# Kernel tuning notes

Measured on AMD Instinct MI355X. Metric: run time of the kernel, lower is better.

The kernel has to match this reference:

```python
import jax, jax.numpy as jnp
import numpy as np

B, T, D, H, K = 8, 4096, 768, 12, 64
EPS_WKV = 1e-9
EPS_GN = 1e-5


def setup_inputs() -> dict:
    key = jax.random.key(0)
    ks = jax.random.split(key, 12)
    x = jax.random.normal(ks[0], (B, T, D), jnp.float32)
    # linear projection weights (torch nn.Linear stores [out, in]; y = x @ W.T)
    W_r = jax.random.normal(ks[1], (D, D), jnp.float32) * 0.02
    W_k = jax.random.normal(ks[2], (D, D), jnp.float32) * 0.02
    W_v = jax.random.normal(ks[3], (D, D), jnp.float32) * 0.02
    W_o = jax.random.normal(ks[4], (D, D), jnp.float32) * 0.02
    time_mix_r = jax.random.uniform(ks[5], (D,), jnp.float32)
    time_mix_k = jax.random.uniform(ks[6], (D,), jnp.float32)
    time_mix_v = jax.random.uniform(ks[7], (D,), jnp.float32)
    # around the module's init values (time_decay ~ -0.075, time_first ~ 0.15 at layer 6/12)
    time_decay = -0.075 + 0.1 * jax.random.normal(ks[8], (H, K), jnp.float32)
    time_first = 0.15 + 0.1 * jax.random.normal(ks[9], (H, K), jnp.float32)
    gn_weight = jnp.ones((D,), jnp.float32)
    gn_bias = jnp.zeros((D,), jnp.float32)
    return {
        "x": x,
        "time_mix_r": time_mix_r, "time_mix_k": time_mix_k, "time_mix_v": time_mix_v,
        "time_decay": time_decay, "time_first": time_first,
        "W_r": W_r, "W_k": W_k, "W_v": W_v, "W_o": W_o,
        "gn_weight": gn_weight, "gn_bias": gn_bias,
    }


def reference(x, time_mix_r, time_mix_k, time_mix_v, time_decay, time_first,
              W_r, W_k, W_v, W_o, gn_weight, gn_bias):
    Bx, Tx, Dx = x.shape
    Hx, Kx = time_decay.shape
    # token-shift: previous timestep (zero-initialized state)
    x_prev = jnp.concatenate([jnp.zeros_like(x[:, :1]), x[:, :-1]], axis=1)
    xr = x * time_mix_r + x_prev * (1.0 - time_mix_r)
    xk = x * time_mix_k + x_prev * (1.0 - time_mix_k)
    xv = x * time_mix_v + x_prev * (1.0 - time_mix_v)
    r = jax.nn.sigmoid(xr @ W_r.T).reshape(Bx, Tx, Hx, Kx)
    k = (xk @ W_k.T).reshape(Bx, Tx, Hx, Kx)
    v = (xv @ W_v.T).reshape(Bx, Tx, Hx, Kx)

    w = jnp.exp(-jnp.exp(time_decay))   # [H,K] decay per channel
    eu = jnp.exp(time_first)            # [H,K] bonus for current token

    def step(carry, kv_t):
        num, den = carry                # each [B,H,K]
        k_t, v_t = kv_t                 # each [B,H,K]
        ek = jnp.exp(k_t)
        wkv = (num + eu * ek * v_t) / (den + eu * ek + EPS_WKV)
        return (num * w + ek * v_t, den * w + ek), wkv

    k_tm = jnp.moveaxis(k, 1, 0)        # [T,B,H,K]
    v_tm = jnp.moveaxis(v, 1, 0)
    init = (jnp.zeros((Bx, Hx, Kx), x.dtype), jnp.zeros((Bx, Hx, Kx), x.dtype))
    _, wkv = jax.lax.scan(step, init, (k_tm, v_tm))
    out = jnp.moveaxis(wkv, 0, 1)       # [B,T,H,K]

    y = r * out                         # [B,T,H,K]
    # torch GroupNorm(H, D) on [B, D, T]: normalize each group over (K channels x T steps)
    mean = y.mean(axis=(1, 3), keepdims=True)
    var = y.var(axis=(1, 3), keepdims=True)
    y = (y - mean) * jax.lax.rsqrt(var + EPS_GN)
    y = y * gn_weight.reshape(1, 1, Hx, Kx) + gn_bias.reshape(1, 1, Hx, Kx)
    return y.reshape(Bx, Tx, Dx) @ W_o.T
```

## Files before the change

kernel.cpp:

```cpp
#include <hip/hip_runtime.h>
#include <hip/hip_bf16.h>
#include <cstdint>

#define B_ 8
#define T_ 4096
#define D_ 768
#define H_ 12
#define M_ (B_*T_)
#define CHUNKS 256
#define CLEN 16
#define WELEM (D_*D_)
#define NCH (B_*H_*64)

typedef __attribute__((ext_vector_type(8))) short bf16x8;
typedef __attribute__((ext_vector_type(4))) float f32x4;

static __device__ __forceinline__ unsigned short f2bf(float f) {
  __hip_bfloat16 h = __float2bfloat16(f);
  return __builtin_bit_cast(unsigned short, h);
}
static __device__ __forceinline__ float bf2f(unsigned short u) {
  unsigned v = ((unsigned)u) << 16;
  return __builtin_bit_cast(float, v);
}

static __device__ __forceinline__ void async16(const void* g, void* l) {
  __builtin_amdgcn_global_load_lds(
      (const __attribute__((address_space(1))) unsigned int*)g,
      (__attribute__((address_space(3))) unsigned int*)l, 16, 0, 0);
}

__global__ __launch_bounds__(256) void zero_out_kernel(float* __restrict__ out, size_t n4) {
  size_t gid = (size_t)blockIdx.x * 256 + threadIdx.x;
  if (gid < n4) *(float4*)(out + gid * 4) = make_float4(0.f, 0.f, 0.f, 0.f);
}

__global__ __launch_bounds__(256) void mix_kernel(
    const float* __restrict__ x, const float* __restrict__ tmr,
    const float* __restrict__ tmk, const float* __restrict__ tmv,
    unsigned short* __restrict__ xr, unsigned short* __restrict__ xk,
    unsigned short* __restrict__ xv) {
  size_t gid = (size_t)blockIdx.x * 256 + threadIdx.x;
  size_t idx4 = gid * 4;
  int d = (int)(idx4 % D_);
  size_t row = idx4 / D_;
  int t = (int)(row & (T_ - 1));
  float4 xc = *(const float4*)(x + idx4);
  float4 xp = make_float4(0.f, 0.f, 0.f, 0.f);
  if (t > 0) xp = *(const float4*)(x + idx4 - D_);
  float4 mr = *(const float4*)(tmr + d);
  float4 mk = *(const float4*)(tmk + d);
  float4 mv = *(const float4*)(tmv + d);
  ushort4 orr, okk, ovv;
  orr.x = f2bf(xc.x*mr.x + xp.x*(1.f-mr.x));
  orr.y = f2bf(xc.y*mr.y + xp.y*(1.f-mr.y));
  orr.z = f2bf(xc.z*mr.z + xp.z*(1.f-mr.z));
  orr.w = f2bf(xc.w*mr.w + xp.w*(1.f-mr.w));
  okk.x = f2bf(xc.x*mk.x + xp.x*(1.f-mk.x));
  okk.y = f2bf(xc.y*mk.y + xp.y*(1.f-mk.y));
  okk.z = f2bf(xc.z*mk.z + xp.z*(1.f-mk.z));
  okk.w = f2bf(xc.w*mk.w + xp.w*(1.f-mk.w));
  ovv.x = f2bf(xc.x*mv.x + xp.x*(1.f-mv.x));
  ovv.y = f2bf(xc.y*mv.y + xp.y*(1.f-mv.y));
  ovv.z = f2bf(xc.z*mv.z + xp.z*(1.f-mv.z));
  ovv.w = f2bf(xc.w*mv.w + xp.w*(1.f-mv.w));
  *(ushort4*)(xr + idx4) = orr;
  *(ushort4*)(xk + idx4) = okk;
  *(ushort4*)(xv + idx4) = ovv;
}

__global__ __launch_bounds__(256) void wconv_kernel(
    const float* __restrict__ a, const float* __restrict__ b,
    const float* __restrict__ c, unsigned short* __restrict__ o) {
  size_t gid = (size_t)blockIdx.x * 256 + threadIdx.x;
  size_t idx4 = gid * 4;
  size_t mi = idx4 / WELEM;
  size_t off = idx4 % WELEM;
  const float* src = (mi == 0) ? a : (mi == 1) ? b : c;
  float4 v = *(const float4*)(src + off);
  ushort4 u;
  u.x = f2bf(v.x); u.y = f2bf(v.y); u.z = f2bf(v.z); u.w = f2bf(v.w);
  *(ushort4*)(o + idx4) = u;
}

template<int ACT, int OBF, int BIAS>
__global__ __launch_bounds__(256, 3) void gemm_nt(
    const unsigned short* __restrict__ A,
    const unsigned short* __restrict__ Bw,
    void* __restrict__ Cv, const float* __restrict__ bias2) {
  __shared__ __align__(16) unsigned short smem[128 * 128];
  const int tid = threadIdx.x;
  const int wave = tid >> 6, lane = tid & 63;
  const int quad = lane >> 4, l16 = lane & 15;

  int nwg = gridDim.x * gridDim.y;
  int lin = blockIdx.y * gridDim.x + blockIdx.x;
  int q = nwg >> 3, r = nwg & 7;
  int xcd = lin & 7, off = lin >> 3;
  int swz = (xcd < r ? xcd * (q + 1) : r * (q + 1) + (xcd - r) * q) + off;
  const int m0 = (swz / gridDim.x) * 128;
  const int n0 = (swz % gridDim.x) * 128;
  const int wm = (wave & 1) * 64, wn = (wave >> 1) * 64;
  const int bb = m0 >> 12;
  const unsigned short* Bp = BIAS ? Bw + (size_t)bb * WELEM : Bw;

  auto stage = [&](int buf, int kb) {
    unsigned short* Ls = smem + buf * (128 * 64);
#pragma unroll
    for (int j = 0; j < 2; ++j) {
      int chunk = j * 256 + tid;
      int row = chunk >> 2, slot = chunk & 3;
      int ks = slot ^ ((row >> 1) & 3);
      async16(A  + ((size_t)(m0 + row)) * D_ + kb + ks * 8, &Ls[chunk * 8]);
      async16(Bp + ((size_t)(n0 + row)) * D_ + kb + ks * 8, &Ls[128 * 32 + chunk * 8]);
    }
  };

  f32x4 acc[4][4] = {};
  const int NT = D_ / 32;

  stage(0, 0);
  __syncthreads();
  int cur = 0;
  for (int t = 0; t < NT; ++t) {
    if (t + 1 < NT) stage(cur ^ 1, (t + 1) * 32);
    const unsigned short* As = smem + cur * (128 * 64);
    const unsigned short* Bs = As + 128 * 32;
    bf16x8 a[4], b[4];
#pragma unroll
    for (int i = 0; i < 4; ++i) {
      int ra = wm + i * 16 + l16;
      a[i] = *(const bf16x8*)&As[ra * 32 + ((quad ^ ((ra >> 1) & 3)) * 8)];
      int rb = wn + i * 16 + l16;
      b[i] = *(const bf16x8*)&Bs[rb * 32 + ((quad ^ ((rb >> 1) & 3)) * 8)];
    }
#pragma unroll
    for (int i = 0; i < 4; ++i)
#pragma unroll
      for (int jj = 0; jj < 4; ++jj)
        acc[i][jj] = __builtin_amdgcn_mfma_f32_16x16x32_bf16(a[i], b[jj], acc[i][jj], 0, 0, 0);
    __syncthreads();
    cur ^= 1;
  }

  if (OBF) {
    unsigned short* Cs = smem;
#pragma unroll
    for (int i = 0; i < 4; ++i) {
#pragma unroll
      for (int jj = 0; jj < 4; ++jj) {
        int col = wn + jj * 16 + l16;
#pragma unroll
        for (int rr = 0; rr < 4; ++rr) {
          int row = wm + i * 16 + quad * 4 + rr;
          float v = acc[i][jj][rr];
          if (ACT == 1) v = 1.f / (1.f + __expf(-v));
          int cg = (col >> 3) ^ (row & 7);
          Cs[row * 128 + cg * 8 + (col & 7)] = f2bf(v);
        }
      }
    }
    __syncthreads();
#pragma unroll
    for (int g = 0; g < 8; ++g) {
      int gi = g * 256 + tid;
      int row = gi >> 4, cg = gi & 15;
      int sg = cg ^ (row & 7);
      bf16x8 vv = *(const bf16x8*)&Cs[row * 128 + sg * 8];
      *(bf16x8*)((unsigned short*)Cv + (size_t)(m0 + row) * D_ + n0 + cg * 8) = vv;
    }
  } else {
#pragma unroll
    for (int i = 0; i < 4; ++i) {
      int rowb = m0 + wm + i * 16 + quad * 4;
#pragma unroll
      for (int jj = 0; jj < 4; ++jj) {
        int col = n0 + wn + jj * 16 + l16;
        float bias = BIAS ? bias2[bb * D_ + col] : 0.f;
#pragma unroll
        for (int rr = 0; rr < 4; ++rr) {
          float v = acc[i][jj][rr] + bias;
          ((float*)Cv)[(size_t)(rowb + rr) * D_ + col] = v;
        }
      }
    }
  }
}

__global__ __launch_bounds__(256) void wkv_pass1(
    const unsigned short* __restrict__ Kb, const unsigned short* __restrict__ Vb,
    const float* __restrict__ td,
    float* __restrict__ sumN, float* __restrict__ sumD) {
  int gid = blockIdx.x * 256 + threadIdx.x;
  int kg = gid & 7;
  int tmp = gid >> 3;
  int h = tmp % H_;
  tmp /= H_;
  int b = tmp % B_;
  int c = tmp / B_;
  const float* tdp = td + h * 64 + kg * 8;
  float w[8], num[8], den[8];
#pragma unroll
  for (int j = 0; j < 8; ++j) {
    w[j] = __expf(-__expf(tdp[j]));
    num[j] = 0.f; den[j] = 0.f;
  }
  size_t base = ((size_t)(b * T_ + c * CLEN)) * D_ + h * 64 + kg * 8;
#pragma unroll 4
  for (int i = 0; i < CLEN; ++i) {
    bf16x8 k8 = *(const bf16x8*)(Kb + base + (size_t)i * D_);
    bf16x8 v8 = *(const bf16x8*)(Vb + base + (size_t)i * D_);
#pragma unroll
    for (int j = 0; j < 8; ++j) {
      float ek = __expf(bf2f((unsigned short)k8[j]));
      num[j] = num[j] * w[j] + ek * bf2f((unsigned short)v8[j]);
      den[j] = den[j] * w[j] + ek;
    }
  }
  int ob = ((c * B_ + b) * H_ + h) * 64 + kg * 8;
  *(float4*)(sumN + ob)     = make_float4(num[0], num[1], num[2], num[3]);
  *(float4*)(sumN + ob + 4) = make_float4(num[4], num[5], num[6], num[7]);
  *(float4*)(sumD + ob)     = make_float4(den[0], den[1], den[2], den[3]);
  *(float4*)(sumD + ob + 4) = make_float4(den[4], den[5], den[6], den[7]);
}

__global__ __launch_bounds__(256) void wkv_pass2(
    const float* __restrict__ sumN, const float* __restrict__ sumD,
    const float* __restrict__ td,
    float* __restrict__ prefN, float* __restrict__ prefD,
    float* __restrict__ gstats) {
  __shared__ float tile[256][64];
  int bid = blockIdx.x;
  if (bid == 0 && threadIdx.x < 192) gstats[threadIdx.x] = 0.f;
  int bh = bid >> 1, qd = bid & 1;
  const float* src = qd ? sumD : sumN;
  float* dst = qd ? prefD : prefN;
  int h = bh % H_;
  int base = bh * 64;
  int t = threadIdx.x;
  {
    int c4 = (t & 15) * 4;
    int rg = t >> 4;
#pragma unroll 4
    for (int i = 0; i < 16; ++i) {
      int row = rg * 16 + i;
      *(float4*)&tile[row][c4] = *(const float4*)&src[(size_t)row * NCH + base + c4];
    }
  }
  __syncthreads();
  int ch = t & 63, g = t >> 6;
  float w = __expf(-__expf(td[h * 64 + ch]));
  float wL = w;
#pragma unroll
  for (int i = 0; i < 4; ++i) wL *= wL;
  float v = 0.f;
  for (int i = 0; i < 64; ++i) {
    int row = g * 64 + i;
    v = v * wL + tile[row][ch];
    tile[row][ch] = v;
  }
  __syncthreads();
  float wL64 = wL;
#pragma unroll
  for (int i = 0; i < 6; ++i) wL64 *= wL64;
  float E = 0.f;
  for (int gp = 0; gp < g; ++gp)
    E = E * wL64 + tile[gp * 64 + 63][ch];
  float f = 1.f;
  for (int i = 0; i < 64; ++i) {
    int row = g * 64 + i;
    float P = (i == 0) ? E : tile[row - 1][ch] + E * f;
    dst[(size_t)row * NCH + base + ch] = P;
    f *= wL;
  }
}

__global__ __launch_bounds__(256) void wkv_pass3(
    const unsigned short* __restrict__ Kb, const unsigned short* __restrict__ Vb,
    unsigned short* __restrict__ RY,
    const float* __restrict__ td, const float* __restrict__ tf,
    const float* __restrict__ prefN, const float* __restrict__ prefD,
    float* __restrict__ gsum, float* __restrict__ gsq) {
  int gid = blockIdx.x * 256 + threadIdx.x;
  int kg = gid & 7;
  int tmp = gid >> 3;
  int h = tmp % H_;
  tmp /= H_;
  int b = tmp % B_;
  int c = tmp / B_;
  const float* tdp = td + h * 64 + kg * 8;
  const float* tfp = tf + h * 64 + kg * 8;
  float w[8], eu[8], num[8], den[8];
  int sb = ((c * B_ + b) * H_ + h) * 64 + kg * 8;
  float4 n0 = *(const float4*)(prefN + sb), n1 = *(const float4*)(prefN + sb + 4);
  float4 d0 = *(const float4*)(prefD + sb), d1 = *(const float4*)(prefD + sb + 4);
  num[0]=n0.x; num[1]=n0.y; num[2]=n0.z; num[3]=n0.w;
  num[4]=n1.x; num[5]=n1.y; num[6]=n1.z; num[7]=n1.w;
  den[0]=d0.x; den[1]=d0.y; den[2]=d0.z; den[3]=d0.w;
  den[4]=d1.x; den[5]=d1.y; den[6]=d1.z; den[7]=d1.w;
#pragma unroll
  for (int j = 0; j < 8; ++j) {
    w[j]  = __expf(-__expf(tdp[j]));
    eu[j] = __expf(tfp[j]);
  }
  size_t base = ((size_t)(b * T_ + c * CLEN)) * D_ + h * 64 + kg * 8;
  float s1 = 0.f, s2 = 0.f;
#pragma unroll 4
  for (int i = 0; i < CLEN; ++i) {
    size_t idx = base + (size_t)i * D_;
    bf16x8 k8 = *(const bf16x8*)(Kb + idx);
    bf16x8 v8 = *(const bf16x8*)(Vb + idx);
    bf16x8 r8 = *(const bf16x8*)(RY + idx);
    bf16x8 y8;
#pragma unroll
    for (int j = 0; j < 8; ++j) {
      float kk = bf2f((unsigned short)k8[j]);
      float vv = bf2f((unsigned short)v8[j]);
      float rr = bf2f((unsigned short)r8[j]);
      float ek = __expf(kk);
      float wkv = __fdividef(num[j] + eu[j] * ek * vv, den[j] + eu[j] * ek + 1e-9f);
      unsigned short ybf = f2bf(rr * wkv);
      y8[j] = (short)ybf;
      float y = bf2f(ybf);
      s1 += y; s2 += y * y;
      num[j] = num[j] * w[j] + ek * vv;
      den[j] = den[j] * w[j] + ek;
    }
    *(bf16x8*)(RY + idx) = y8;
  }
#pragma unroll
  for (int off = 4; off; off >>= 1) {
    s1 += __shfl_xor(s1, off);
    s2 += __shfl_xor(s2, off);
  }
  if (kg == 0) {
    atomicAdd(&gsum[b * H_ + h], s1);
    atomicAdd(&gsq [b * H_ + h], s2);
  }
}

__global__ __launch_bounds__(256) void woprep_kernel(
    const float* __restrict__ Wo, const float* __restrict__ gsum,
    const float* __restrict__ gsq, const float* __restrict__ gw,
    unsigned short* __restrict__ Wob) {
  int blk = blockIdx.x;
  int b = blk / (WELEM / 1024);
  size_t off = (size_t)(blk % (WELEM / 1024)) * 1024 + threadIdx.x * 4;
  int d = (int)(off % D_);
  int g = b * H_ + (d >> 6);
  const float inv = 1.f / (float)(T_ * 64);
  float mean = gsum[g] * inv;
  float var = gsq[g] * inv - mean * mean;
  float rstd = rsqrtf(var + 1e-5f);
  float4 wo = *(const float4*)(Wo + off);
  float4 gwv = *(const float4*)(gw + d);
  ushort4 o;
  o.x = f2bf(wo.x * rstd * gwv.x);
  o.y = f2bf(wo.y * rstd * gwv.y);
  o.z = f2bf(wo.z * rstd * gwv.z);
  o.w = f2bf(wo.w * rstd * gwv.w);
  *(ushort4*)(Wob + (size_t)b * WELEM + off) = o;
}

__global__ __launch_bounds__(256) void bias2_kernel(
    const float* __restrict__ Wo, const float* __restrict__ gsum,
    const float* __restrict__ gsq, const float* __restrict__ gw,
    const float* __restrict__ gb, float* __restrict__ bias2) {
  int blk = blockIdx.x;
  int b = blk / 12, nb = (blk % 12) * 64;
  int lane = threadIdx.x & 63, wv = threadIdx.x >> 6;
  const float inv = 1.f / (float)(T_ * 64);
  float cB[12];
#pragma unroll
  for (int j = 0; j < 12; ++j) {
    int d = lane + 64 * j;
    int g = b * H_ + j;
    float mean = gsum[g] * inv;
    float var = gsq[g] * inv - mean * mean;
    float rstd = rsqrtf(var + 1e-5f);
    cB[j] = gb[d] - mean * rstd * gw[d];
  }
  for (int n = nb + wv * 16, e = n + 16; n < e; ++n) {
    float s = 0.f;
#pragma unroll
    for (int j = 0; j < 12; ++j)
      s += cB[j] * Wo[(size_t)n * D_ + lane + 64 * j];
#pragma unroll
    for (int off = 32; off; off >>= 1) s += __shfl_down(s, off);
    if (lane == 0) bias2[b * D_ + n] = s;
  }
}

extern "C" void kernel_launch(void* const* d_in, const int* in_sizes, int n_in,
                              void* d_out, int out_size, void* d_ws, size_t ws_size,
                              hipStream_t stream) {
  (void)in_sizes; (void)n_in;
  const float* x   = (const float*)d_in[0];
  const float* tmr = (const float*)d_in[1];
  const float* tmk = (const float*)d_in[2];
  const float* tmv = (const float*)d_in[3];
  const float* td  = (const float*)d_in[4];
  const float* tf  = (const float*)d_in[5];
  const float* Wr  = (const float*)d_in[6];
  const float* Wk  = (const float*)d_in[7];
  const float* Wv  = (const float*)d_in[8];
  const float* Wo  = (const float*)d_in[9];
  const float* gw  = (const float*)d_in[10];
  const float* gb  = (const float*)d_in[11];
  float* out = (float*)d_out;

  constexpr size_t MD = (size_t)M_ * D_;
  constexpr size_t NEED = 4 * (MD * 2)
                        + (size_t)4 * WELEM * 2
                        + 4 * ((size_t)CHUNKS * NCH * 4)
                        + 1024;
  if (ws_size < NEED) {
    zero_out_kernel<<<(int)((MD / 4 + 255) / 256), 256, 0, stream>>>(out, MD / 4);
    return;
  }

  char* ws = (char*)d_ws;
  unsigned short* XR = (unsigned short*)ws; ws += MD * 2;
  unsigned short* XK = (unsigned short*)ws; ws += MD * 2;
  unsigned short* XV = (unsigned short*)ws; ws += MD * 2;
  unsigned short* Rb = (unsigned short*)ws; ws += MD * 2;
  unsigned short* Wb = (unsigned short*)ws; ws += (size_t)4 * WELEM * 2;
  float* sumN  = (float*)ws; ws += (size_t)CHUNKS * NCH * 4;
  float* sumD  = (float*)ws; ws += (size_t)CHUNKS * NCH * 4;
  float* prefN = (float*)ws; ws += (size_t)CHUNKS * NCH * 4;
  float* prefD = (float*)ws; ws += (size_t)CHUNKS * NCH * 4;
  float* gstats = (float*)ws; ws += 1024;
  unsigned short* Kb = XR;
  unsigned short* Vb = XK;
  unsigned short* Wob = (unsigned short*)sumN;
  float* bias2 = prefN;

  mix_kernel<<<(int)(MD / 1024), 256, 0, stream>>>(x, tmr, tmk, tmv, XR, XK, XV);
  wconv_kernel<<<(3 * WELEM / 4) / 256, 256, 0, stream>>>(Wr, Wk, Wv, Wb);

  dim3 ggrid(D_ / 128, M_ / 128);
  gemm_nt<1, 1, 0><<<ggrid, 256, 0, stream>>>(XR, Wb,             Rb, nullptr);
  gemm_nt<0, 1, 0><<<ggrid, 256, 0, stream>>>(XK, Wb + WELEM,     Kb, nullptr);
  gemm_nt<0, 1, 0><<<ggrid, 256, 0, stream>>>(XV, Wb + 2 * WELEM, Vb, nullptr);

  wkv_pass1<<<(CHUNKS * NCH / 8) / 256, 256, 0, stream>>>(Kb, Vb, td, sumN, sumD);
  wkv_pass2<<<192, 256, 0, stream>>>(sumN, sumD, td, prefN, prefD, gstats);
  wkv_pass3<<<(CHUNKS * NCH / 8) / 256, 256, 0, stream>>>(Kb, Vb, Rb, td, tf,
                                                          prefN, prefD, gstats, gstats + 96);

  woprep_kernel<<<8 * (WELEM / 1024), 256, 0, stream>>>(Wo, gstats, gstats + 96, gw, Wob);
  bias2_kernel<<<96, 256, 0, stream>>>(Wo, gstats, gstats + 96, gw, gb, bias2);

  gemm_nt<0, 0, 1><<<ggrid, 256, 0, stream>>>(Rb, Wob, out, bias2);
}
```

Baseline: 515.8 us.

## Enlarge GEMM block tile to 256x128 with 128x64 per-wave tiles

After: 552.4 us. 1.07x slower.

```diff
diff --git a/kernel.cpp b/kernel.cpp
--- a/kernel.cpp
+++ b/kernel.cpp
@@ -84,11 +84,11 @@
 }
 
 template<int ACT, int OBF, int BIAS>
-__global__ __launch_bounds__(256, 3) void gemm_nt(
+__global__ __launch_bounds__(256, 2) void gemm_nt(
     const unsigned short* __restrict__ A,
     const unsigned short* __restrict__ Bw,
     void* __restrict__ Cv, const float* __restrict__ bias2) {
-  __shared__ __align__(16) unsigned short smem[128 * 128];
+  __shared__ __align__(16) unsigned short smem[2][12288];
   const int tid = threadIdx.x;
   const int wave = tid >> 6, lane = tid & 63;
   const int quad = lane >> 4, l16 = lane & 15;
@@ -98,25 +98,32 @@
   int q = nwg >> 3, r = nwg & 7;
   int xcd = lin & 7, off = lin >> 3;
   int swz = (xcd < r ? xcd * (q + 1) : r * (q + 1) + (xcd - r) * q) + off;
-  const int m0 = (swz / gridDim.x) * 128;
+  const int m0 = (swz / gridDim.x) * 256;
   const int n0 = (swz % gridDim.x) * 128;
-  const int wm = (wave & 1) * 64, wn = (wave >> 1) * 64;
+  const int wr = wave >> 1, wc = wave & 1;
   const int bb = m0 >> 12;
   const unsigned short* Bp = BIAS ? Bw + (size_t)bb * WELEM : Bw;
 
   auto stage = [&](int buf, int kb) {
-    unsigned short* Ls = smem + buf * (128 * 64);
+    unsigned short* As = smem[buf];
+    unsigned short* Bs = smem[buf] + 8192;
+#pragma unroll
+    for (int j = 0; j < 4; ++j) {
+      int chunk = j * 256 + tid;
+      int row = chunk >> 2, slot = chunk & 3;
+      int ks = slot ^ ((row >> 1) & 3);
+      async16(A + ((size_t)(m0 + row)) * D_ + kb + ks * 8, &As[chunk * 8]);
+    }
 #pragma unroll
     for (int j = 0; j < 2; ++j) {
       int chunk = j * 256 + tid;
       int row = chunk >> 2, slot = chunk & 3;
       int ks = slot ^ ((row >> 1) & 3);
-      async16(A  + ((size_t)(m0 + row)) * D_ + kb + ks * 8, &Ls[chunk * 8]);
-      async16(Bp + ((size_t)(n0 + row)) * D_ + kb + ks * 8, &Ls[128 * 32 + chunk * 8]);
+      async16(Bp + ((size_t)(n0 + row)) * D_ + kb + ks * 8, &Bs[chunk * 8]);
     }
   };
 
-  f32x4 acc[4][4] = {};
+  f32x4 acc[8][4] = {};
   const int NT = D_ / 32;
 
   stage(0, 0);
@@ -124,18 +131,21 @@
   int cur = 0;
   for (int t = 0; t < NT; ++t) {
     if (t + 1 < NT) stage(cur ^ 1, (t + 1) * 32);
-    const unsigned short* As = smem + cur * (128 * 64);
-    const unsigned short* Bs = As + 128 * 32;
-    bf16x8 a[4], b[4];
-#pragma unroll
-    for (int i = 0; i < 4; ++i) {
-      int ra = wm + i * 16 + l16;
+    const unsigned short* As = smem[cur];
+    const unsigned short* Bs = smem[cur] + 8192;
+    bf16x8 a[8], b[4];
+#pragma unroll
+    for (int i = 0; i < 8; ++i) {
+      int ra = wr * 128 + i * 16 + l16;
       a[i] = *(const bf16x8*)&As[ra * 32 + ((quad ^ ((ra >> 1) & 3)) * 8)];
-      int rb = wn + i * 16 + l16;
-      b[i] = *(const bf16x8*)&Bs[rb * 32 + ((quad ^ ((rb >> 1) & 3)) * 8)];
-    }
-#pragma unroll
-    for (int i = 0; i < 4; ++i)
+    }
+#pragma unroll
+    for (int j = 0; j < 4; ++j) {
+      int rb = wc * 64 + j * 16 + l16;
+      b[j] = *(const bf16x8*)&Bs[rb * 32 + ((quad ^ ((rb >> 1) & 3)) * 8)];
+    }
+#pragma unroll
+    for (int i = 0; i < 8; ++i)
 #pragma unroll
       for (int jj = 0; jj < 4; ++jj)
         acc[i][jj] = __builtin_amdgcn_mfma_f32_16x16x32_bf16(a[i], b[jj], acc[i][jj], 0, 0, 0);
@@ -144,38 +154,44 @@
   }
 
   if (OBF) {
-    unsigned short* Cs = smem;
-#pragma unroll
-    for (int i = 0; i < 4; ++i) {
-#pragma unroll
-      for (int jj = 0; jj < 4; ++jj) {
-        int col = wn + jj * 16 + l16;
-#pragma unroll
-        for (int rr = 0; rr < 4; ++rr) {
-          int row = wm + i * 16 + quad * 4 + rr;
-          float v = acc[i][jj][rr];
-          if (ACT == 1) v = 1.f / (1.f + __expf(-v));
-          int cg = (col >> 3) ^ (row & 7);
-          Cs[row * 128 + cg * 8 + (col & 7)] = f2bf(v);
+    unsigned short* Cs = smem[0];
+#pragma unroll
+    for (int p = 0; p < 2; ++p) {
+      if (wr == p) {
+#pragma unroll
+        for (int i = 0; i < 8; ++i) {
+#pragma unroll
+          for (int jj = 0; jj < 4; ++jj) {
+            int col = wc * 64 + jj * 16 + l16;
+#pragma unroll
+            for (int rr = 0; rr < 4; ++rr) {
+              int row = i * 16 + quad * 4 + rr;
+              float v = acc[i][jj][rr];
+              if (ACT == 1) v = 1.f / (1.f + __expf(-v));
+              int cg = (col >> 3) ^ (row & 7);
+              Cs[row * 128 + cg * 8 + (col & 7)] = f2bf(v);
+            }
+          }
         }
       }
-    }
-    __syncthreads();
-#pragma unroll
-    for (int g = 0; g < 8; ++g) {
-      int gi = g * 256 + tid;
-      int row = gi >> 4, cg = gi & 15;
-      int sg = cg ^ (row & 7);
-      bf16x8 vv = *(const bf16x8*)&Cs[row * 128 + sg * 8];
-      *(bf16x8*)((unsigned short*)Cv + (size_t)(m0 + row) * D_ + n0 + cg * 8) = vv;
+      __syncthreads();
+#pragma unroll
+      for (int g = 0; g < 8; ++g) {
+        int gi = g * 256 + tid;
+        int row = gi >> 4, cg = gi & 15;
+        int sg = cg ^ (row & 7);
+        bf16x8 vv = *(const bf16x8*)&Cs[row * 128 + sg * 8];
+        *(bf16x8*)((unsigned short*)Cv + (size_t)(m0 + p * 128 + row) * D_ + n0 + cg * 8) = vv;
+      }
+      __syncthreads();
     }
   } else {
 #pragma unroll
-    for (int i = 0; i < 4; ++i) {
-      int rowb = m0 + wm + i * 16 + quad * 4;
+    for (int i = 0; i < 8; ++i) {
+      int rowb = m0 + wr * 128 + i * 16 + quad * 4;
 #pragma unroll
       for (int jj = 0; jj < 4; ++jj) {
-        int col = n0 + wn + jj * 16 + l16;
+        int col = n0 + wc * 64 + jj * 16 + l16;
         float bias = BIAS ? bias2[bb * D_ + col] : 0.f;
 #pragma unroll
         for (int rr = 0; rr < 4; ++rr) {
@@ -438,7 +454,7 @@
   mix_kernel<<<(int)(MD / 1024), 256, 0, stream>>>(x, tmr, tmk, tmv, XR, XK, XV);
   wconv_kernel<<<(3 * WELEM / 4) / 256, 256, 0, stream>>>(Wr, Wk, Wv, Wb);
 
-  dim3 ggrid(D_ / 128, M_ / 128);
+  dim3 ggrid(D_ / 128, M_ / 256);
   gemm_nt<1, 1, 0><<<ggrid, 256, 0, stream>>>(XR, Wb,             Rb, nullptr);
   gemm_nt<0, 1, 0><<<ggrid, 256, 0, stream>>>(XK, Wb + WELEM,     Kb, nullptr);
   gemm_nt<0, 1, 0><<<ggrid, 256, 0, stream>>>(XV, Wb + 2 * WELEM, Vb, nullptr);
```
